# Kernel optimization log

Hardware: AMD Instinct MI355X
Metric: run time of the kernel (lower is better)

Reference implementation:

```python
import jax, jax.numpy as jnp
import numpy as np

EPS = 1e-8  # torch CosineSimilarity eps


def _cosine_sim_matrix(x, y):
    # x: [Nx, D], y: [Ny, D] -> [Nx, Ny] cosine similarity via normalized GEMM
    xn = x / jnp.maximum(jnp.linalg.norm(x, axis=-1, keepdims=True), EPS)
    yn = y / jnp.maximum(jnp.linalg.norm(y, axis=-1, keepdims=True), EPS)
    return xn @ yn.T


def setup_inputs() -> dict:
    key = jax.random.key(0)
    k1, k2, k3, k4 = jax.random.split(key, 4)
    N, D, C = 4096, 512, 100
    inst_embed = jax.random.normal(k1, (N, D), dtype=jnp.float32)
    proxy = jax.random.normal(k2, (N, D), dtype=jnp.float32)
    # binary positive-selection mask per class over the batch
    negative_mask = (jax.random.uniform(k3, (C, N)) > 0.5).astype(jnp.float32)
    labels = jax.random.randint(k4, (N,), 0, C, dtype=jnp.int64)
    temperature = jnp.float32(0.1)
    margin = jnp.float32(0.0)
    return {"inst_embed": inst_embed, "proxy": proxy,
            "negative_mask": negative_mask, "labels": labels,
            "temperature": temperature, "margin": margin}


def reference(inst_embed, proxy, negative_mask, labels, temperature, margin):
    # [N, N] similarity matrices
    p2i = _cosine_sim_matrix(proxy, inst_embed)
    i2i = _cosine_sim_matrix(inst_embed, inst_embed)
    p2i_zone = jnp.exp((p2i - margin) / temperature)
    i2i_zone = jnp.exp((i2i - margin) / temperature)
    mask = negative_mask[labels]  # [N, N]
    p2i_num = (p2i_zone * mask).sum(axis=1)
    i2i_num = (i2i_zone * mask).sum(axis=1)
    p2i_den = p2i_zone.sum(axis=1)
    i2i_den = i2i_zone.sum(axis=1)
    p2i_loss = -jnp.log(temperature * (p2i_num / p2i_den)).mean()
    i2i_loss = -jnp.log(temperature * (i2i_num / i2i_den)).mean()
    return p2i_loss + i2i_loss
```

## Files before the change

### kernel.cpp

```cpp
#include <hip/hip_runtime.h>
#include <hip/hip_bf16.h>

#define D_DIM 512
#define KSTEPS 16
#define BM 64
#define BN 64
#define GRIDY 4

typedef __bf16 bf16x8 __attribute__((ext_vector_type(8)));
typedef float  f32x4  __attribute__((ext_vector_type(4)));

__device__ __forceinline__ unsigned short f2bf_rne(float x) {
    unsigned int u = __float_as_uint(x);
    u += 0x7FFFu + ((u >> 16) & 1u);
    return (unsigned short)(u >> 16);
}

__global__ __launch_bounds__(128) void normalize_rows(
    const float* __restrict__ inst, const float* __restrict__ proxy,
    unsigned short* __restrict__ instb, unsigned short* __restrict__ proxyb, int N)
{
    int row = blockIdx.x;
    const float* src;
    unsigned short* dst;
    if (row < N) { src = inst  + (size_t)row * D_DIM;        dst = instb  + (size_t)row * D_DIM; }
    else         { src = proxy + (size_t)(row - N) * D_DIM;  dst = proxyb + (size_t)(row - N) * D_DIM; }
    int t = threadIdx.x;
    float4 v = ((const float4*)src)[t];
    float ss = v.x*v.x + v.y*v.y + v.z*v.z + v.w*v.w;
    #pragma unroll
    for (int off = 32; off > 0; off >>= 1) ss += __shfl_down(ss, off, 64);
    __shared__ float wss[2];
    if ((t & 63) == 0) wss[t >> 6] = ss;
    __syncthreads();
    float inv = 1.0f / fmaxf(sqrtf(wss[0] + wss[1]), 1e-8f);
    ushort4 o;
    o.x = f2bf_rne(v.x * inv); o.y = f2bf_rne(v.y * inv);
    o.z = f2bf_rne(v.z * inv); o.w = f2bf_rne(v.w * inv);
    ((ushort4*)dst)[t] = o;
}

__global__ __launch_bounds__(256, 2) void fused_scores(
    const unsigned short* __restrict__ instb,
    const unsigned short* __restrict__ proxyb,
    const float* __restrict__ negmask,
    const int*  __restrict__ labels,
    const float* __restrict__ temp_p,
    const float* __restrict__ margin_p,
    float* __restrict__ nd,
    int N, int colsPerBlock)
{
    __shared__ unsigned short Bt[BN * D_DIM];

    const int tid  = threadIdx.x;
    const int lane = tid & 63;
    const int wave = tid >> 6;
    const int quad = lane >> 4;
    const int l16  = lane & 15;

    const int Rbase  = blockIdx.x * BM + wave * 16;
    const bool isP2I = (Rbase < N);
    const unsigned short* Aptr = isP2I ? (proxyb + (size_t)Rbase * D_DIM)
                                       : (instb  + (size_t)(Rbase - N) * D_DIM);
    const int rowLocal = isP2I ? Rbase : (Rbase - N);

    const float temp  = *temp_p;
    const float scale = 1.44269504088896340736f / temp;
    const float bias  = -(*margin_p) * scale;

    bf16x8 Afrag[KSTEPS];
    {
        const unsigned short* arow = Aptr + (size_t)l16 * D_DIM + quad * 8;
        #pragma unroll
        for (int ks = 0; ks < KSTEPS; ks++)
            Afrag[ks] = *(const bf16x8*)(arow + ks * 32);
    }

    int lab[4];
    #pragma unroll
    for (int r = 0; r < 4; r++) lab[r] = labels[rowLocal + quad * 4 + r];

    float numAcc[4] = {0.f,0.f,0.f,0.f};
    float denAcc[4] = {0.f,0.f,0.f,0.f};

    const int j0base = blockIdx.y * colsPerBlock;
    for (int jt = 0; jt < colsPerBlock; jt += BN) {
        const int j0 = j0base + jt;
        __syncthreads();
        #pragma unroll
        for (int it = 0; it < (BN * (D_DIM/8)) / 256; it++) {
            int c   = tid + it * 256;
            int br  = c >> 6;
            int ch  = c & 63;
            int chs = ch ^ (br & 7);
            float4 v = ((const float4*)(instb + (size_t)(j0 + br) * D_DIM))[ch];
            *(float4*)&Bt[br * D_DIM + chs * 8] = v;
        }
        __syncthreads();

        f32x4 acc[4] = {};
        #pragma unroll
        for (int ks = 0; ks < KSTEPS; ks++) {
            #pragma unroll
            for (int cg = 0; cg < 4; cg++) {
                int rB  = cg * 16 + l16;
                int chs = (ks * 4 + quad) ^ (rB & 7);
                bf16x8 b = *(const bf16x8*)&Bt[rB * D_DIM + chs * 8];
                acc[cg] = __builtin_amdgcn_mfma_f32_16x16x32_bf16(Afrag[ks], b, acc[cg], 0, 0, 0);
            }
        }

        #pragma unroll
        for (int cg = 0; cg < 4; cg++) {
            int j = j0 + cg * 16 + l16;
            #pragma unroll
            for (int r = 0; r < 4; r++) {
                float zone = exp2f(acc[cg][r] * scale + bias);
                denAcc[r] += zone;
                float m = negmask[(size_t)lab[r] * N + j];
                numAcc[r] += zone * m;
            }
        }
    }

    #pragma unroll
    for (int r = 0; r < 4; r++) {
        float n = numAcc[r], d = denAcc[r];
        #pragma unroll
        for (int off = 8; off > 0; off >>= 1) {
            n += __shfl_down(n, off, 16);
            d += __shfl_down(d, off, 16);
        }
        if (l16 == 0) {
            float* numArr = nd + (isP2I ? 0 : 2 * N);
            float* denArr = numArr + N;
            atomicAdd(&numArr[rowLocal + quad * 4 + r], n);
            atomicAdd(&denArr[rowLocal + quad * 4 + r], d);
        }
    }
}

__global__ __launch_bounds__(256) void loss_reduce(
    const float* __restrict__ nd, const float* __restrict__ temp_p,
    float* __restrict__ out, int N)
{
    const float t = *temp_p;
    float s = 0.f;
    for (int i = threadIdx.x; i < N; i += 256) {
        s -= logf(t * nd[i]         / nd[N + i]);
        s -= logf(t * nd[2 * N + i] / nd[3 * N + i]);
    }
    #pragma unroll
    for (int off = 32; off > 0; off >>= 1) s += __shfl_down(s, off, 64);
    __shared__ float wss[4];
    if ((threadIdx.x & 63) == 0) wss[threadIdx.x >> 6] = s;
    __syncthreads();
    if (threadIdx.x == 0) out[0] = (wss[0] + wss[1] + wss[2] + wss[3]) / (float)N;
}

extern "C" void kernel_launch(void* const* d_in, const int* in_sizes, int n_in,
                              void* d_out, int out_size, void* d_ws, size_t ws_size,
                              hipStream_t stream)
{
    const float* inst     = (const float*)d_in[0];
    const float* proxy    = (const float*)d_in[1];
    const float* negmask  = (const float*)d_in[2];
    const int*   labels   = (const int*)d_in[3];
    const float* temp_p   = (const float*)d_in[4];
    const float* margin_p = (const float*)d_in[5];
    float* out = (float*)d_out;

    const int N = in_sizes[3];

    unsigned short* instb  = (unsigned short*)d_ws;
    unsigned short* proxyb = instb + (size_t)N * D_DIM;
    float* nd = (float*)(proxyb + (size_t)N * D_DIM);

    hipMemsetAsync(nd, 0, sizeof(float) * 4 * N, stream);
    normalize_rows<<<2 * N, 128, 0, stream>>>(inst, proxy, instb, proxyb, N);
    dim3 grid(2 * N / BM, GRIDY);
    fused_scores<<<grid, 256, 0, stream>>>(instb, proxyb, negmask, labels,
                                           temp_p, margin_p, nd, N, N / GRIDY);
    loss_reduce<<<1, 256, 0, stream>>>(nd, temp_p, out, N);
}
```

Before: 142.3 us.

## Double per-wave row tile and store B tile in MFMA-fragment order in LDS

Each wave now computes 32 rows instead of 16, so every B fragment read from LDS feeds two MFMAs and a block covers 128 rows. The B tile is laid out in LDS in the exact per-lane fragment order, which replaces the XOR swizzle with contiguous conflict-free reads. GRIDY is doubled to 8 so the grid keeps enough blocks. In exchange the kernel holds twice as many A-fragment and accumulator registers, which may lower occupancy or cause spills, and issues more atomics per block.

```diff
diff --git a/kernel.cpp b/kernel.cpp
--- a/kernel.cpp
+++ b/kernel.cpp
@@ -3,9 +3,9 @@
 
 #define D_DIM 512
 #define KSTEPS 16
-#define BM 64
+#define BM 128
 #define BN 64
-#define GRIDY 4
+#define GRIDY 8
 
 typedef __bf16 bf16x8 __attribute__((ext_vector_type(8)));
 typedef float  f32x4  __attribute__((ext_vector_type(4)));
@@ -58,7 +58,7 @@
     const int quad = lane >> 4;
     const int l16  = lane & 15;
 
-    const int Rbase  = blockIdx.x * BM + wave * 16;
+    const int Rbase  = blockIdx.x * BM + wave * 32;
     const bool isP2I = (Rbase < N);
     const unsigned short* Aptr = isP2I ? (proxyb + (size_t)Rbase * D_DIM)
                                        : (instb  + (size_t)(Rbase - N) * D_DIM);
@@ -68,45 +68,48 @@
     const float scale = 1.44269504088896340736f / temp;
     const float bias  = -(*margin_p) * scale;
 
-    bf16x8 Afrag[KSTEPS];
-    {
-        const unsigned short* arow = Aptr + (size_t)l16 * D_DIM + quad * 8;
+    bf16x8 Afrag[2][KSTEPS];
+    #pragma unroll
+    for (int s = 0; s < 2; s++) {
+        const unsigned short* arow = Aptr + (size_t)(s * 16 + l16) * D_DIM + quad * 8;
         #pragma unroll
         for (int ks = 0; ks < KSTEPS; ks++)
-            Afrag[ks] = *(const bf16x8*)(arow + ks * 32);
+            Afrag[s][ks] = *(const bf16x8*)(arow + ks * 32);
     }
 
-    int lab[4];
+    int lab[2][4];
     #pragma unroll
-    for (int r = 0; r < 4; r++) lab[r] = labels[rowLocal + quad * 4 + r];
+    for (int s = 0; s < 2; s++)
+        #pragma unroll
+        for (int r = 0; r < 4; r++)
+            lab[s][r] = labels[rowLocal + s * 16 + quad * 4 + r];
 
-    float numAcc[4] = {0.f,0.f,0.f,0.f};
-    float denAcc[4] = {0.f,0.f,0.f,0.f};
+    float numAcc[2][4] = {};
+    float denAcc[2][4] = {};
 
     const int j0base = blockIdx.y * colsPerBlock;
     for (int jt = 0; jt < colsPerBlock; jt += BN) {
         const int j0 = j0base + jt;
         __syncthreads();
         #pragma unroll
-        for (int it = 0; it < (BN * (D_DIM/8)) / 256; it++) {
-            int c   = tid + it * 256;
-            int br  = c >> 6;
-            int ch  = c & 63;
-            int chs = ch ^ (br & 7);
-            float4 v = ((const float4*)(instb + (size_t)(j0 + br) * D_DIM))[ch];
-            *(float4*)&Bt[br * D_DIM + chs * 8] = v;
+        for (int it = 0; it < 16; it++) {
+            int dc_hi = it * 4 + wave;
+            int ks = dc_hi >> 2;
+            int cg = dc_hi & 3;
+            const unsigned short* src =
+                instb + (size_t)(j0 + cg * 16 + l16) * D_DIM + ks * 32 + quad * 8;
+            *(bf16x8*)&Bt[(size_t)(dc_hi * 64 + lane) * 8] = *(const bf16x8*)src;
         }
         __syncthreads();
 
-        f32x4 acc[4] = {};
+        f32x4 acc[2][4] = {};
         #pragma unroll
         for (int ks = 0; ks < KSTEPS; ks++) {
             #pragma unroll
             for (int cg = 0; cg < 4; cg++) {
-                int rB  = cg * 16 + l16;
-                int chs = (ks * 4 + quad) ^ (rB & 7);
-                bf16x8 b = *(const bf16x8*)&Bt[rB * D_DIM + chs * 8];
-                acc[cg] = __builtin_amdgcn_mfma_f32_16x16x32_bf16(Afrag[ks], b, acc[cg], 0, 0, 0);
+                bf16x8 b = *(const bf16x8*)&Bt[(size_t)(((ks * 4 + cg) * 64) + lane) * 8];
+                acc[0][cg] = __builtin_amdgcn_mfma_f32_16x16x32_bf16(Afrag[0][ks], b, acc[0][cg], 0, 0, 0);
+                acc[1][cg] = __builtin_amdgcn_mfma_f32_16x16x32_bf16(Afrag[1][ks], b, acc[1][cg], 0, 0, 0);
             }
         }
 
@@ -114,28 +117,35 @@
         for (int cg = 0; cg < 4; cg++) {
             int j = j0 + cg * 16 + l16;
             #pragma unroll
-            for (int r = 0; r < 4; r++) {
-                float zone = exp2f(acc[cg][r] * scale + bias);
-                denAcc[r] += zone;
-                float m = negmask[(size_t)lab[r] * N + j];
-                numAcc[r] += zone * m;
+            for (int s = 0; s < 2; s++) {
+                #pragma unroll
+                for (int r = 0; r < 4; r++) {
+                    float zone = exp2f(acc[s][cg][r] * scale + bias);
+                    denAcc[s][r] += zone;
+                    float m = negmask[(size_t)lab[s][r] * N + j];
+                    numAcc[s][r] += zone * m;
+                }
             }
         }
     }
 
+    float* numArr = nd + (isP2I ? 0 : 2 * N);
+    float* denArr = numArr + N;
     #pragma unroll
-    for (int r = 0; r < 4; r++) {
-        float n = numAcc[r], d = denAcc[r];
+    for (int s = 0; s < 2; s++) {
         #pragma unroll
-        for (int off = 8; off > 0; off >>= 1) {
-            n += __shfl_down(n, off, 16);
-            d += __shfl_down(d, off, 16);
-        }
-        if (l16 == 0) {
-            float* numArr = nd + (isP2I ? 0 : 2 * N);
-            float* denArr = numArr + N;
-            atomicAdd(&numArr[rowLocal + quad * 4 + r], n);
-            atomicAdd(&denArr[rowLocal + quad * 4 + r], d);
+        for (int r = 0; r < 4; r++) {
+            float n = numAcc[s][r], d = denAcc[s][r];
+            #pragma unroll
+            for (int off = 8; off > 0; off >>= 1) {
+                n += __shfl_down(n, off, 16);
+                d += __shfl_down(d, off, 16);
+            }
+            if (l16 == 0) {
+                int row = rowLocal + s * 16 + quad * 4 + r;
+                atomicAdd(&numArr[row], n);
+                atomicAdd(&denArr[row], d);
+            }
         }
     }
 }
```

After: 170.5 us. +19.8%, slower.

## Retile fused score GEMM to 256x128 blocks with async global-to-LDS k-slices

Applied to the files above, without the earlier changes.

Replaces the old scheme, where each wave kept a full 512-wide A fragment in registers and streamed 64-column B tiles. Each block now computes a 256x128 output tile with a K-loop of 64-wide slices. Every slice is staged through LDS with global_load_lds async copies laid out in MFMA fragment order. Each wave holds a 4x8 grid of accumulators, giving more reuse per loaded byte, and applies exp, mask and reduction once at the end. The normalize kernel now handles one row per wave and writes inst and proxy into one contiguous buffer. The change adds register pressure from 32 accumulators and a sync per k-slice with no double buffering, which may limit occupancy and overlap.

```diff
diff --git a/kernel.cpp b/kernel.cpp
--- a/kernel.cpp
+++ b/kernel.cpp
@@ -2,13 +2,17 @@
 #include <hip/hip_bf16.h>
 
 #define D_DIM 512
-#define KSTEPS 16
-#define BM 64
-#define BN 64
-#define GRIDY 4
 
 typedef __bf16 bf16x8 __attribute__((ext_vector_type(8)));
 typedef float  f32x4  __attribute__((ext_vector_type(4)));
+
+typedef unsigned int u32;
+typedef __attribute__((address_space(1))) const u32 gl_u32;
+typedef __attribute__((address_space(3))) u32 lds_u32;
+
+__device__ __forceinline__ void async_copy16(const void* gsrc, void* ldst) {
+    __builtin_amdgcn_global_load_lds((gl_u32*)gsrc, (lds_u32*)ldst, 16, 0, 0);
+}
 
 __device__ __forceinline__ unsigned short f2bf_rne(float x) {
     unsigned int u = __float_as_uint(x);
@@ -16,41 +20,40 @@
     return (unsigned short)(u >> 16);
 }
 
-__global__ __launch_bounds__(128) void normalize_rows(
+__global__ __launch_bounds__(256) void normalize_rows(
     const float* __restrict__ inst, const float* __restrict__ proxy,
-    unsigned short* __restrict__ instb, unsigned short* __restrict__ proxyb, int N)
+    unsigned short* __restrict__ out, int N)
 {
-    int row = blockIdx.x;
-    const float* src;
-    unsigned short* dst;
-    if (row < N) { src = inst  + (size_t)row * D_DIM;        dst = instb  + (size_t)row * D_DIM; }
-    else         { src = proxy + (size_t)(row - N) * D_DIM;  dst = proxyb + (size_t)(row - N) * D_DIM; }
-    int t = threadIdx.x;
-    float4 v = ((const float4*)src)[t];
-    float ss = v.x*v.x + v.y*v.y + v.z*v.z + v.w*v.w;
+    int row  = blockIdx.x * 4 + (threadIdx.x >> 6);
+    int lane = threadIdx.x & 63;
+    const float* src = (row < N) ? inst + (size_t)row * D_DIM
+                                 : proxy + (size_t)(row - N) * D_DIM;
+    float4 v0 = ((const float4*)src)[lane];
+    float4 v1 = ((const float4*)src)[lane + 64];
+    float ss = v0.x*v0.x + v0.y*v0.y + v0.z*v0.z + v0.w*v0.w
+             + v1.x*v1.x + v1.y*v1.y + v1.z*v1.z + v1.w*v1.w;
     #pragma unroll
-    for (int off = 32; off > 0; off >>= 1) ss += __shfl_down(ss, off, 64);
-    __shared__ float wss[2];
-    if ((t & 63) == 0) wss[t >> 6] = ss;
-    __syncthreads();
-    float inv = 1.0f / fmaxf(sqrtf(wss[0] + wss[1]), 1e-8f);
-    ushort4 o;
-    o.x = f2bf_rne(v.x * inv); o.y = f2bf_rne(v.y * inv);
-    o.z = f2bf_rne(v.z * inv); o.w = f2bf_rne(v.w * inv);
-    ((ushort4*)dst)[t] = o;
+    for (int off = 1; off < 64; off <<= 1) ss += __shfl_xor(ss, off, 64);
+    float inv = 1.0f / fmaxf(sqrtf(ss), 1e-8f);
+    unsigned short* dst = out + (size_t)row * D_DIM;
+    ushort4 o0, o1;
+    o0.x = f2bf_rne(v0.x*inv); o0.y = f2bf_rne(v0.y*inv);
+    o0.z = f2bf_rne(v0.z*inv); o0.w = f2bf_rne(v0.w*inv);
+    o1.x = f2bf_rne(v1.x*inv); o1.y = f2bf_rne(v1.y*inv);
+    o1.z = f2bf_rne(v1.z*inv); o1.w = f2bf_rne(v1.w*inv);
+    ((ushort4*)dst)[lane]      = o0;
+    ((ushort4*)dst)[lane + 64] = o1;
 }
 
 __global__ __launch_bounds__(256, 2) void fused_scores(
-    const unsigned short* __restrict__ instb,
-    const unsigned short* __restrict__ proxyb,
+    const unsigned short* __restrict__ emb,
     const float* __restrict__ negmask,
     const int*  __restrict__ labels,
     const float* __restrict__ temp_p,
     const float* __restrict__ margin_p,
-    float* __restrict__ nd,
-    int N, int colsPerBlock)
+    float* __restrict__ nd, int N)
 {
-    __shared__ unsigned short Bt[BN * D_DIM];
+    __shared__ unsigned short TILE[48 * D_DIM / 8 * 8];
 
     const int tid  = threadIdx.x;
     const int lane = tid & 63;
@@ -58,84 +61,79 @@
     const int quad = lane >> 4;
     const int l16  = lane & 15;
 
-    const int Rbase  = blockIdx.x * BM + wave * 16;
+    const int Cbase = blockIdx.x * 128;
+    const int Rbase = blockIdx.y * 256;
     const bool isP2I = (Rbase < N);
-    const unsigned short* Aptr = isP2I ? (proxyb + (size_t)Rbase * D_DIM)
-                                       : (instb  + (size_t)(Rbase - N) * D_DIM);
-    const int rowLocal = isP2I ? Rbase : (Rbase - N);
+    const int AbaseEmb = isP2I ? (N + Rbase) : (Rbase - N);
+    const int rowLoc0  = (isP2I ? Rbase : (Rbase - N)) + wave * 64;
 
     const float temp  = *temp_p;
     const float scale = 1.44269504088896340736f / temp;
     const float bias  = -(*margin_p) * scale;
 
-    bf16x8 Afrag[KSTEPS];
-    {
-        const unsigned short* arow = Aptr + (size_t)l16 * D_DIM + quad * 8;
-        #pragma unroll
-        for (int ks = 0; ks < KSTEPS; ks++)
-            Afrag[ks] = *(const bf16x8*)(arow + ks * 32);
+    unsigned fragOff[12];
+    #pragma unroll
+    for (int i = 0; i < 12; i++) {
+        int f = wave * 12 + i;
+        int sub = (f < 32) ? (f >> 1) : ((f - 32) >> 1);
+        int ks  = f & 1;
+        int rowE = (f < 32) ? (AbaseEmb + sub * 16 + l16)
+                            : (Cbase    + sub * 16 + l16);
+        fragOff[i] = (unsigned)((rowE * D_DIM + ks * 32 + quad * 8) * 2);
     }
 
-    int lab[4];
-    #pragma unroll
-    for (int r = 0; r < 4; r++) lab[r] = labels[rowLocal + quad * 4 + r];
+    f32x4 acc[4][8] = {};
 
-    float numAcc[4] = {0.f,0.f,0.f,0.f};
-    float denAcc[4] = {0.f,0.f,0.f,0.f};
-
-    const int j0base = blockIdx.y * colsPerBlock;
-    for (int jt = 0; jt < colsPerBlock; jt += BN) {
-        const int j0 = j0base + jt;
+    for (int kit = 0; kit < 8; kit++) {
         __syncthreads();
         #pragma unroll
-        for (int it = 0; it < (BN * (D_DIM/8)) / 256; it++) {
-            int c   = tid + it * 256;
-            int br  = c >> 6;
-            int ch  = c & 63;
-            int chs = ch ^ (br & 7);
-            float4 v = ((const float4*)(instb + (size_t)(j0 + br) * D_DIM))[ch];
-            *(float4*)&Bt[br * D_DIM + chs * 8] = v;
-        }
+        for (int i = 0; i < 12; i++)
+            async_copy16((const char*)emb + fragOff[i] + kit * 128,
+                         &TILE[(wave * 12 + i) * 512]);
         __syncthreads();
-
-        f32x4 acc[4] = {};
         #pragma unroll
-        for (int ks = 0; ks < KSTEPS; ks++) {
+        for (int ks = 0; ks < 2; ks++) {
+            bf16x8 a[4], b[8];
             #pragma unroll
-            for (int cg = 0; cg < 4; cg++) {
-                int rB  = cg * 16 + l16;
-                int chs = (ks * 4 + quad) ^ (rB & 7);
-                bf16x8 b = *(const bf16x8*)&Bt[rB * D_DIM + chs * 8];
-                acc[cg] = __builtin_amdgcn_mfma_f32_16x16x32_bf16(Afrag[ks], b, acc[cg], 0, 0, 0);
-            }
-        }
-
-        #pragma unroll
-        for (int cg = 0; cg < 4; cg++) {
-            int j = j0 + cg * 16 + l16;
+            for (int mi = 0; mi < 4; mi++)
+                a[mi] = *(const bf16x8*)&TILE[((wave * 4 + mi) * 2 + ks) * 512 + lane * 8];
             #pragma unroll
-            for (int r = 0; r < 4; r++) {
-                float zone = exp2f(acc[cg][r] * scale + bias);
-                denAcc[r] += zone;
-                float m = negmask[(size_t)lab[r] * N + j];
-                numAcc[r] += zone * m;
-            }
+            for (int nt = 0; nt < 8; nt++)
+                b[nt] = *(const bf16x8*)&TILE[(32 + nt * 2 + ks) * 512 + lane * 8];
+            #pragma unroll
+            for (int mi = 0; mi < 4; mi++)
+                #pragma unroll
+                for (int nt = 0; nt < 8; nt++)
+                    acc[mi][nt] = __builtin_amdgcn_mfma_f32_16x16x32_bf16(
+                        a[mi], b[nt], acc[mi][nt], 0, 0, 0);
         }
     }
 
+    float* numArr = nd + (isP2I ? 0 : 2 * N);
+    float* denArr = numArr + N;
     #pragma unroll
-    for (int r = 0; r < 4; r++) {
-        float n = numAcc[r], d = denAcc[r];
+    for (int mi = 0; mi < 4; mi++) {
         #pragma unroll
-        for (int off = 8; off > 0; off >>= 1) {
-            n += __shfl_down(n, off, 16);
-            d += __shfl_down(d, off, 16);
-        }
-        if (l16 == 0) {
-            float* numArr = nd + (isP2I ? 0 : 2 * N);
-            float* denArr = numArr + N;
-            atomicAdd(&numArr[rowLocal + quad * 4 + r], n);
-            atomicAdd(&denArr[rowLocal + quad * 4 + r], d);
+        for (int r = 0; r < 4; r++) {
+            int row = rowLoc0 + mi * 16 + quad * 4 + r;
+            int lab = labels[row];
+            const float* mrow = negmask + (size_t)lab * N + Cbase + l16;
+            float den = 0.f, num = 0.f;
+            #pragma unroll
+            for (int nt = 0; nt < 8; nt++) {
+                float zone = exp2f(acc[mi][nt][r] * scale + bias);
+                den += zone;
+                num += zone * mrow[nt * 16];
+            }
+            #pragma unroll
+            for (int off = 8; off > 0; off >>= 1) {
+                num += __shfl_down(num, off, 16);
+                den += __shfl_down(den, off, 16);
+            }
+            if (l16 == 0) {
+                atomicAdd(&numArr[row], num);
+                atomicAdd(&denArr[row], den);
+            }
         }
     }
 }
@@ -172,14 +170,13 @@
 
     const int N = in_sizes[3];
 
-    unsigned short* instb  = (unsigned short*)d_ws;
-    unsigned short* proxyb = instb + (size_t)N * D_DIM;
-    float* nd = (float*)(proxyb + (size_t)N * D_DIM);
+    unsigned short* emb = (unsigned short*)d_ws;
+    float* nd = (float*)(emb + (size_t)2 * N * D_DIM);
 
     hipMemsetAsync(nd, 0, sizeof(float) * 4 * N, stream);
-    normalize_rows<<<2 * N, 128, 0, stream>>>(inst, proxy, instb, proxyb, N);
-    dim3 grid(2 * N / BM, GRIDY);
-    fused_scores<<<grid, 256, 0, stream>>>(instb, proxyb, negmask, labels,
-                                           temp_p, margin_p, nd, N, N / GRIDY);
+    normalize_rows<<<2 * N / 4, 256, 0, stream>>>(inst, proxy, emb, N);
+    dim3 grid(N / 128, 2 * N / 256);
+    fused_scores<<<grid, 256, 0, stream>>>(emb, negmask, labels,
+                                           temp_p, margin_p, nd, N);
     loss_reduce<<<1, 256, 0, stream>>>(nd, temp_p, out, N);
 }
```

Result: slower. 151.2 us (+6.2%).

## Fold memset and loss reduction into neighbouring kernels, pre-fragment B tile in LDS

Applied to the files above, without the earlier changes.

Zeroing of the accumulators moves into the normalize kernel, which now processes four rows per block with one wave per row. The final loss reduction moves into the scores kernel through a last-block ticket counter, which removes two launches. The B tile is now staged in LDS already laid out in MFMA fragment order, so the inner loop reads contiguous per-lane vectors with no XOR swizzle. The costs are a threadfence plus a global atomic ticket per block, and a single serial tail block that performs the final reduction.

```diff
diff --git a/kernel.cpp b/kernel.cpp
--- a/kernel.cpp
+++ b/kernel.cpp
@@ -16,41 +16,46 @@
     return (unsigned short)(u >> 16);
 }
 
-__global__ __launch_bounds__(128) void normalize_rows(
+__global__ __launch_bounds__(256) void normalize_rows(
     const float* __restrict__ inst, const float* __restrict__ proxy,
-    unsigned short* __restrict__ instb, unsigned short* __restrict__ proxyb, int N)
+    unsigned short* __restrict__ out, float* __restrict__ nd, int N)
 {
-    int row = blockIdx.x;
-    const float* src;
-    unsigned short* dst;
-    if (row < N) { src = inst  + (size_t)row * D_DIM;        dst = instb  + (size_t)row * D_DIM; }
-    else         { src = proxy + (size_t)(row - N) * D_DIM;  dst = proxyb + (size_t)(row - N) * D_DIM; }
-    int t = threadIdx.x;
-    float4 v = ((const float4*)src)[t];
-    float ss = v.x*v.x + v.y*v.y + v.z*v.z + v.w*v.w;
+    if (blockIdx.x < 16) {
+        for (int i = blockIdx.x * 256 + threadIdx.x; i < 4 * N + 16; i += 4096)
+            nd[i] = 0.f;
+    }
+    int row  = blockIdx.x * 4 + (threadIdx.x >> 6);
+    int lane = threadIdx.x & 63;
+    const float* src = (row < N) ? inst + (size_t)row * D_DIM
+                                 : proxy + (size_t)(row - N) * D_DIM;
+    float4 v0 = ((const float4*)src)[lane];
+    float4 v1 = ((const float4*)src)[lane + 64];
+    float ss = v0.x*v0.x + v0.y*v0.y + v0.z*v0.z + v0.w*v0.w
+             + v1.x*v1.x + v1.y*v1.y + v1.z*v1.z + v1.w*v1.w;
     #pragma unroll
-    for (int off = 32; off > 0; off >>= 1) ss += __shfl_down(ss, off, 64);
-    __shared__ float wss[2];
-    if ((t & 63) == 0) wss[t >> 6] = ss;
-    __syncthreads();
-    float inv = 1.0f / fmaxf(sqrtf(wss[0] + wss[1]), 1e-8f);
-    ushort4 o;
-    o.x = f2bf_rne(v.x * inv); o.y = f2bf_rne(v.y * inv);
-    o.z = f2bf_rne(v.z * inv); o.w = f2bf_rne(v.w * inv);
-    ((ushort4*)dst)[t] = o;
+    for (int off = 1; off < 64; off <<= 1) ss += __shfl_xor(ss, off, 64);
+    float inv = 1.0f / fmaxf(sqrtf(ss), 1e-8f);
+    unsigned short* dst = out + (size_t)row * D_DIM;
+    ushort4 o0, o1;
+    o0.x = f2bf_rne(v0.x*inv); o0.y = f2bf_rne(v0.y*inv);
+    o0.z = f2bf_rne(v0.z*inv); o0.w = f2bf_rne(v0.w*inv);
+    o1.x = f2bf_rne(v1.x*inv); o1.y = f2bf_rne(v1.y*inv);
+    o1.z = f2bf_rne(v1.z*inv); o1.w = f2bf_rne(v1.w*inv);
+    ((ushort4*)dst)[lane]      = o0;
+    ((ushort4*)dst)[lane + 64] = o1;
 }
 
 __global__ __launch_bounds__(256, 2) void fused_scores(
-    const unsigned short* __restrict__ instb,
-    const unsigned short* __restrict__ proxyb,
+    const unsigned short* __restrict__ emb,
     const float* __restrict__ negmask,
     const int*  __restrict__ labels,
     const float* __restrict__ temp_p,
     const float* __restrict__ margin_p,
     float* __restrict__ nd,
-    int N, int colsPerBlock)
+    float* __restrict__ out, int N, int colsPerBlock)
 {
     __shared__ unsigned short Bt[BN * D_DIM];
+    __shared__ bool amLast;
 
     const int tid  = threadIdx.x;
     const int lane = tid & 63;
@@ -60,8 +65,8 @@
 
     const int Rbase  = blockIdx.x * BM + wave * 16;
     const bool isP2I = (Rbase < N);
-    const unsigned short* Aptr = isP2I ? (proxyb + (size_t)Rbase * D_DIM)
-                                       : (instb  + (size_t)(Rbase - N) * D_DIM);
+    const unsigned short* Aptr = isP2I ? (emb + (size_t)(N + Rbase) * D_DIM)
+                                       : (emb + (size_t)(Rbase - N) * D_DIM);
     const int rowLocal = isP2I ? Rbase : (Rbase - N);
 
     const float temp  = *temp_p;
@@ -88,13 +93,13 @@
         const int j0 = j0base + jt;
         __syncthreads();
         #pragma unroll
-        for (int it = 0; it < (BN * (D_DIM/8)) / 256; it++) {
-            int c   = tid + it * 256;
-            int br  = c >> 6;
-            int ch  = c & 63;
-            int chs = ch ^ (br & 7);
-            float4 v = ((const float4*)(instb + (size_t)(j0 + br) * D_DIM))[ch];
-            *(float4*)&Bt[br * D_DIM + chs * 8] = v;
+        for (int it = 0; it < 16; it++) {
+            int f  = it * 4 + wave;
+            int ks = f >> 2;
+            int cg = f & 3;
+            const unsigned short* src =
+                emb + (size_t)(j0 + cg * 16 + l16) * D_DIM + ks * 32 + quad * 8;
+            *(bf16x8*)&Bt[f * 512 + lane * 8] = *(const bf16x8*)src;
         }
         __syncthreads();
 
@@ -103,9 +108,7 @@
         for (int ks = 0; ks < KSTEPS; ks++) {
             #pragma unroll
             for (int cg = 0; cg < 4; cg++) {
-                int rB  = cg * 16 + l16;
-                int chs = (ks * 4 + quad) ^ (rB & 7);
-                bf16x8 b = *(const bf16x8*)&Bt[rB * D_DIM + chs * 8];
+                bf16x8 b = *(const bf16x8*)&Bt[(ks * 4 + cg) * 512 + lane * 8];
                 acc[cg] = __builtin_amdgcn_mfma_f32_16x16x32_bf16(Afrag[ks], b, acc[cg], 0, 0, 0);
             }
         }
@@ -123,6 +126,8 @@
         }
     }
 
+    float* numArr = nd + (isP2I ? 0 : 2 * N);
+    float* denArr = numArr + N;
     #pragma unroll
     for (int r = 0; r < 4; r++) {
         float n = numAcc[r], d = denAcc[r];
@@ -132,30 +137,34 @@
             d += __shfl_down(d, off, 16);
         }
         if (l16 == 0) {
-            float* numArr = nd + (isP2I ? 0 : 2 * N);
-            float* denArr = numArr + N;
             atomicAdd(&numArr[rowLocal + quad * 4 + r], n);
             atomicAdd(&denArr[rowLocal + quad * 4 + r], d);
         }
     }
-}
 
-__global__ __launch_bounds__(256) void loss_reduce(
-    const float* __restrict__ nd, const float* __restrict__ temp_p,
-    float* __restrict__ out, int N)
-{
-    const float t = *temp_p;
-    float s = 0.f;
-    for (int i = threadIdx.x; i < N; i += 256) {
-        s -= logf(t * nd[i]         / nd[N + i]);
-        s -= logf(t * nd[2 * N + i] / nd[3 * N + i]);
+    __threadfence();
+    if (tid == 0) {
+        unsigned* ticket = (unsigned*)(nd + 4 * N);
+        unsigned t = atomicAdd(ticket, 1u);
+        amLast = (t == gridDim.x * gridDim.y - 1);
     }
-    #pragma unroll
-    for (int off = 32; off > 0; off >>= 1) s += __shfl_down(s, off, 64);
-    __shared__ float wss[4];
-    if ((threadIdx.x & 63) == 0) wss[threadIdx.x >> 6] = s;
     __syncthreads();
-    if (threadIdx.x == 0) out[0] = (wss[0] + wss[1] + wss[2] + wss[3]) / (float)N;
+    if (amLast) {
+        float s = 0.f;
+        for (int i = tid; i < N; i += 256) {
+            float pn = __hip_atomic_load(&nd[i],         __ATOMIC_RELAXED, __HIP_MEMORY_SCOPE_AGENT);
+            float pd = __hip_atomic_load(&nd[N + i],     __ATOMIC_RELAXED, __HIP_MEMORY_SCOPE_AGENT);
+            float in_ = __hip_atomic_load(&nd[2 * N + i], __ATOMIC_RELAXED, __HIP_MEMORY_SCOPE_AGENT);
+            float id_ = __hip_atomic_load(&nd[3 * N + i], __ATOMIC_RELAXED, __HIP_MEMORY_SCOPE_AGENT);
+            s -= logf(temp * pn / pd) + logf(temp * in_ / id_);
+        }
+        #pragma unroll
+        for (int off = 32; off > 0; off >>= 1) s += __shfl_down(s, off, 64);
+        __shared__ float wss[4];
+        if ((tid & 63) == 0) wss[tid >> 6] = s;
+        __syncthreads();
+        if (tid == 0) out[0] = (wss[0] + wss[1] + wss[2] + wss[3]) / (float)N;
+    }
 }
 
 extern "C" void kernel_launch(void* const* d_in, const int* in_sizes, int n_in,
@@ -172,14 +181,11 @@
 
     const int N = in_sizes[3];
 
-    unsigned short* instb  = (unsigned short*)d_ws;
-    unsigned short* proxyb = instb + (size_t)N * D_DIM;
-    float* nd = (float*)(proxyb + (size_t)N * D_DIM);
+    unsigned short* emb = (unsigned short*)d_ws;
+    float* nd = (float*)(emb + (size_t)2 * N * D_DIM);
 
-    hipMemsetAsync(nd, 0, sizeof(float) * 4 * N, stream);
-    normalize_rows<<<2 * N, 128, 0, stream>>>(inst, proxy, instb, proxyb, N);
+    normalize_rows<<<2 * N / 4, 256, 0, stream>>>(inst, proxy, emb, nd, N);
     dim3 grid(2 * N / BM, GRIDY);
-    fused_scores<<<grid, 256, 0, stream>>>(instb, proxyb, negmask, labels,
-                                           temp_p, margin_p, nd, N, N / GRIDY);
-    loss_reduce<<<1, 256, 0, stream>>>(nd, temp_p, out, N);
+    fused_scores<<<grid, 256, 0, stream>>>(emb, negmask, labels,
+                                           temp_p, margin_p, nd, out, N, N / GRIDY);
 }
```

After: 185.7 us. 1.3x slower.
